# Kernel tuning notes

Hardware: AMD Instinct MI355X
Metric: run time of the kernel (lower is better)

## Reference

```python
import jax, jax.numpy as jnp
import numpy as np

B, D, CTX, H = 8192, 64, 256, 512  # batch, latent dim (made.nin), context dim, MADE hidden


def _masks(D, H):
    """Standard MADE natural-ordering masks (Germain et al. 2015)."""
    m0 = np.arange(1, D + 1)                 # input degrees 1..D
    mh = (np.arange(H) % (D - 1)) + 1        # hidden degrees 1..D-1
    M1 = (mh[:, None] >= m0[None, :]).astype(np.float32)   # (H, D)
    M2 = (mh[:, None] >= mh[None, :]).astype(np.float32)   # (H, H)
    mo = np.concatenate([m0, m0])            # outputs = [means; pre_scales]
    Mo = (mo[:, None] > mh[None, :]).astype(np.float32)    # (2D, H)
    return jnp.asarray(M1), jnp.asarray(M2), jnp.asarray(Mo)


def setup_inputs() -> dict:
    key = jax.random.key(0)
    ks = jax.random.split(key, 7)
    s = 0.05
    return {
        "context": jax.random.normal(ks[0], (B, CTX), jnp.float32),
        "eps": jax.random.normal(ks[1], (B, D), jnp.float32),  # reparameterization noise
        "W1": jax.random.normal(ks[2], (H, D), jnp.float32) * s,
        "b1": jnp.zeros((H,), jnp.float32),
        "Wc": jax.random.normal(ks[3], (H, CTX), jnp.float32) * s,
        "W2": jax.random.normal(ks[4], (H, H), jnp.float32) * s,
        "b2": jnp.zeros((H,), jnp.float32),
        "Wo": jax.random.normal(ks[5], (2 * D, H), jnp.float32) * s,
        "bo": jnp.zeros((2 * D,), jnp.float32),
    }


def reference(context, eps, W1, b1, Wc, W2, b2, Wo, bo):
    """AutoRegressiveDistribution.rsample (gaussian): D sequential MADE forwards,
    each extracting column i of (mu, softplus(pre_scale)) and sampling z_i."""
    M1, M2, Mo = _masks(D, H)
    W1m, W2m, Wom = (W1 * M1).T, (W2 * M2).T, (Wo * Mo).T
    ctx_h = context @ Wc.T  # context projection is constant across steps

    def step(z, i):
        h = jax.nn.relu(z @ W1m + ctx_h + b1)   # (B, H)
        h = jax.nn.relu(h @ W2m + b2)           # (B, H)
        out = h @ Wom + bo                      # (B, 2D): [means | pre_scales]
        mu_i = out[:, i]
        scale_i = jax.nn.softplus(out[:, D + i])
        z_i = mu_i + scale_i * eps[:, i]        # Normal(mu, scale).rsample()
        z = z.at[:, i].set(z_i)
        return z, (mu_i, scale_i)

    z0 = jnp.zeros((context.shape[0], D), context.dtype)
    z, (mus, scales) = jax.lax.scan(step, z0, jnp.arange(D))
    # state = (z_sample, mu_inferred, scale_inferred), each (B, D)
    return z, mus.T, scales.T
```

## Files before the change

kernel.cpp:

```cpp
#include <hip/hip_runtime.h>
#include <math.h>


typedef float f2 __attribute__((ext_vector_type(2)));

#define Bn 8192
#define Dn 64
#define CTXn 256
#define Hn 512
#define Rn 16

#define WQ_SZ  (64 * 512 * 12)
#define WOQ_SZ (64 * 64 * 20)
#define WCP_SZ (CTXn * Hn)

#define BARRIER() do {                                      \
    asm volatile("s_waitcnt lgkmcnt(0)" ::: "memory");      \
    __builtin_amdgcn_s_barrier();                           \
    asm volatile("" ::: "memory");                          \
  } while (0)

__device__ __forceinline__ int perm_of(int p, int* degout) {
  int k, t;
  if (p < 72) { k = p / 9 + 1; t = p - (k - 1) * 9; }
  else        { int pp = p - 72; k = pp / 8 + 9; t = pp - (k - 9) * 8; }
  *degout = k;
  return (k - 1) + 63 * t;
}
__device__ __forceinline__ int inv_perm(int h) {
  int i = h % 63;
  int t = h / 63;
  int base = (i < 9) ? 9 * i : 72 + 8 * (i - 8);
  return base + t;
}

#define R0e 262144
#define R1e (R0e + 32768)
#define R2e (R1e + 65536)
#define R3e (R2e + 131072)
#define R4e (R3e + 35840)
#define R5e (R4e + 1024)
__global__ void prep_kernel(const float* __restrict__ W1, const float* __restrict__ Wc,
                            const float* __restrict__ W2, const float* __restrict__ Wo,
                            const float* __restrict__ b1, const float* __restrict__ b2,
                            float* __restrict__ Wq, float* __restrict__ Woq,
                            float* __restrict__ WcpT, float* __restrict__ b1p,
                            float* __restrict__ b2p) {
  int idx = blockIdx.x * 256 + threadIdx.x;
  if (idx < R0e) {
    int hq = idx >> 9, hp = idx & 511;
    int i = hp % 63, e = hp / 63;
    Wq[i * 6144 + inv_perm(hq) * 12 + e] = W2[idx];
  } else if (idx < R1e) {
    int jj = idx - R0e;
    int hq = jj >> 6, i = jj & 63;
    Wq[i * 6144 + inv_perm(hq) * 12 + 9] = W1[jj];
  } else if (idx < R2e) {
    int jj = idx - R1e;
    int o = jj >> 9, hp = jj & 511;
    int i = hp % 63, p = hp / 63;
    int j = o & 63, half = o >> 6;
    Woq[i * 1280 + j * 20 + half * 10 + p] = Wo[jj];
  } else if (idx < R3e) {
    int jj = idx - R2e;
    int hq = jj >> 8, cc = jj & 255;
    int p = inv_perm(hq);
    int slot = (p < 256) ? (2 * p) : (2 * (p - 256) + 1);
    WcpT[cc * 512 + slot] = Wc[jj];
  } else if (idx < R4e) {
    int z = idx - R3e;
    if (z < 28672) {
      int i = 8 + (z >> 9), q = z & 511;
      Wq[i * 6144 + q * 12 + 8] = 0.f;
    } else {
      int z2 = z - 28672;
      int i = 8 + (z2 >> 7), r = z2 & 127;
      int j = r & 63, half = r >> 6;
      Woq[i * 1280 + j * 20 + half * 10 + 8] = 0.f;
    }
  } else if (idx < R5e) {
    int z = idx - R4e;
    if (z < 512) {
      int dq; int hq = perm_of(z, &dq);
      b1p[z] = b1[hq];
    } else {
      int q = z - 512;
      int dq; int hq = perm_of(q, &dq);
      b2p[q] = b2[hq];
    }
  }
}

__global__ __launch_bounds__(256, 2)
void made_pk_kernel(
    const float* __restrict__ context, const float* __restrict__ WcpT,
    const float* __restrict__ b1p,
    const float* __restrict__ Wq, const float* __restrict__ Woq,
    const float* __restrict__ b2p, const float* __restrict__ bo,
    const float* __restrict__ eps, float* __restrict__ out) {
  __shared__ __align__(16) float ctxR[Rn][264];
  __shared__ __align__(16) float zcur[16];
  __shared__ __align__(16) float h1g[9][16];
  __shared__ __align__(16) float h2g[9][16];

  int t = threadIdx.x;
  int b0 = blockIdx.x * Rn;
  int rp = t >> 6, l = t & 63;
  int q0 = t, q1 = t + 256;

  int g0 = ((q0 < 72) ? q0 / 9 + 1 : (q0 - 72) / 8 + 9) - 1;
  int g1 = ((q1 - 72) / 8 + 9) - 1;
  int qm = t | 63;
  int gm0s = __builtin_amdgcn_readfirstlane(
      ((qm < 72) ? qm / 9 + 1 : (qm - 72) / 8 + 9) - 1);
  int gm1s = __builtin_amdgcn_readfirstlane(((qm + 256 - 72) / 8 + 9) - 1);

  #pragma unroll
  for (int r = 0; r < Rn; ++r)
    ctxR[r][t] = context[(b0 + r) * CTXn + t];
  BARRIER();

  f2 accu[16];
  {
    f2 bias = (f2){b1p[q0], b1p[q1]};
    #pragma unroll
    for (int r = 0; r < 16; ++r) accu[r] = bias;
  }
  {
    const float* wc = WcpT + 2 * t;
    #pragma clang loop unroll(disable)
    for (int c4 = 0; c4 < CTXn / 4; ++c4) {
      f2 wv0 = *(const f2*)&wc[0];
      f2 wv1 = *(const f2*)&wc[Hn];
      f2 wv2 = *(const f2*)&wc[2 * Hn];
      f2 wv3 = *(const f2*)&wc[3 * Hn];
      wc += 4 * Hn;
      #pragma unroll
      for (int hf = 0; hf < 2; ++hf) {
        float4 x[8];
        #pragma unroll
        for (int r = 0; r < 8; ++r) x[r] = *(const float4*)&ctxR[8 * hf + r][4 * c4];
        #pragma unroll
        for (int r = 0; r < 8; ++r) {
          accu[8 * hf + r] += (f2){x[r].x, x[r].x} * wv0;
          accu[8 * hf + r] += (f2){x[r].y, x[r].y} * wv1;
          accu[8 * hf + r] += (f2){x[r].z, x[r].z} * wv2;
          accu[8 * hf + r] += (f2){x[r].w, x[r].w} * wv3;
        }
      }
    }
  }

  f2 a10[8], a11[8], a20[8], a21[8];
  #pragma unroll
  for (int r2 = 0; r2 < 8; ++r2) {
    a10[r2] = (f2){accu[2 * r2].x, accu[2 * r2 + 1].x};
    a11[r2] = (f2){accu[2 * r2].y, accu[2 * r2 + 1].y};
  }
  {
    float bb0 = b2p[q0], bb1 = b2p[q1];
    #pragma unroll
    for (int r2 = 0; r2 < 8; ++r2) {
      a20[r2] = (f2){bb0, bb0};
      a21[r2] = (f2){bb1, bb1};
    }
  }

  f2 ocA[2], ocB[2];
  ocA[0] = ocA[1] = (f2){bo[l], bo[l]};
  ocB[0] = ocB[1] = (f2){bo[l + 64], bo[l + 64]};
  int r0 = b0 + 4 * rp;
  f2 ez01 = (f2){eps[(r0 + 0) * Dn + l], eps[(r0 + 1) * Dn + l]};
  f2 ez23 = (f2){eps[(r0 + 2) * Dn + l], eps[(r0 + 3) * Dn + l]};
  f2 zs01 = (f2){0.f, 0.f}, zs23 = zs01;
  f2 mus01 = zs01, mus23 = zs01, scs01 = zs01, scs23 = zs01;

  const float* wq0p = Wq + (size_t)q0 * 12;
  const float* wq1p = Wq + (size_t)q1 * 12;
  const float* wopp = Woq + (size_t)l * 20;

  #pragma clang loop unroll(disable)
  for (int i = 0; i < Dn; ++i) {
    if (l == i) {
      f2 p01 = ocB[0], p23 = ocB[1];
      float s0 = fmaxf(p01.x, 0.f) + __logf(1.f + __expf(-fabsf(p01.x)));
      float s1 = fmaxf(p01.y, 0.f) + __logf(1.f + __expf(-fabsf(p01.y)));
      float s2 = fmaxf(p23.x, 0.f) + __logf(1.f + __expf(-fabsf(p23.x)));
      float s3 = fmaxf(p23.y, 0.f) + __logf(1.f + __expf(-fabsf(p23.y)));
      f2 sc01 = (f2){s0, s1}, sc23 = (f2){s2, s3};
      f2 z01 = ocA[0] + sc01 * ez01;
      f2 z23 = ocA[1] + sc23 * ez23;
      float4 zq = {z01.x, z01.y, z23.x, z23.y};
      *(float4*)&zcur[4 * rp] = zq;
      zs01 = z01; zs23 = z23;
      mus01 = ocA[0]; mus23 = ocA[1];
      scs01 = sc01; scs23 = sc23;
    }
    BARRIER();

    int sb = (i < 8) ? 9 * i : 8 * i + 8;
    bool liveB = (i <= gm1s);
    bool liveA = (i <= gm0s);
    float4 A1c0, A1c1, A1c2, A0c0, A0c1, A0c2;
    if (liveB) {
      const float4* a4 = (const float4*)wq1p;
      A1c0 = a4[0]; A1c1 = a4[1]; A1c2 = a4[2];
      if (liveA) {
        const float4* b4 = (const float4*)wq0p;
        A0c0 = b4[0]; A0c1 = b4[1]; A0c2 = b4[2];
      }
      float4 za = *(const float4*)&zcur[0];
      float4 zb = *(const float4*)&zcur[4];
      float4 zc = *(const float4*)&zcur[8];
      float4 zd = *(const float4*)&zcur[12];
      f2 zz[8] = {(f2){za.x, za.y}, (f2){za.z, za.w},
                  (f2){zb.x, zb.y}, (f2){zb.z, zb.w},
                  (f2){zc.x, zc.y}, (f2){zc.z, zc.w},
                  (f2){zd.x, zd.y}, (f2){zd.z, zd.w}};
      {
        f2 wv = (f2){A1c2.y, A1c2.y};
        #pragma unroll
        for (int r2 = 0; r2 < 8; ++r2) a11[r2] += wv * zz[r2];
        if (g1 == i) {
          int pp = q1 - sb;
          #pragma unroll
          for (int s = 0; s < 4; ++s) {
            float4 h = {fmaxf(a11[2 * s].x, 0.f), fmaxf(a11[2 * s].y, 0.f),
                        fmaxf(a11[2 * s + 1].x, 0.f), fmaxf(a11[2 * s + 1].y, 0.f)};
            *(float4*)&h1g[pp][4 * s] = h;
          }
        }
      }
      if (liveA) {
        f2 wv = (f2){A0c2.y, A0c2.y};
        #pragma unroll
        for (int r2 = 0; r2 < 8; ++r2) a10[r2] += wv * zz[r2];
        if (g0 == i) {
          int pp = q0 - sb;
          #pragma unroll
          for (int s = 0; s < 4; ++s) {
            float4 h = {fmaxf(a10[2 * s].x, 0.f), fmaxf(a10[2 * s].y, 0.f),
                        fmaxf(a10[2 * s + 1].x, 0.f), fmaxf(a10[2 * s + 1].y, 0.f)};
            *(float4*)&h1g[pp][4 * s] = h;
          }
        }
      }
    }
    BARRIER();

    const float4* w4 = (const float4*)wopp;
    float4 B0 = w4[0], B1 = w4[1], B2_ = w4[2], B3 = w4[3], B4 = w4[4];

    if (liveB) {
      float wA1[9] = {A1c0.x, A1c0.y, A1c0.z, A1c0.w,
                      A1c1.x, A1c1.y, A1c1.z, A1c1.w, A1c2.x};
      if (liveA) {
        float wA0[9] = {A0c0.x, A0c0.y, A0c0.z, A0c0.w,
                        A0c1.x, A0c1.y, A0c1.z, A0c1.w, A0c2.x};
        #pragma unroll
        for (int p = 0; p < 9; ++p) {
          float4 ha = *(const float4*)&h1g[p][0];
          float4 hb = *(const float4*)&h1g[p][4];
          float4 hc = *(const float4*)&h1g[p][8];
          float4 hd = *(const float4*)&h1g[p][12];
          f2 h[8] = {(f2){ha.x, ha.y}, (f2){ha.z, ha.w},
                     (f2){hb.x, hb.y}, (f2){hb.z, hb.w},
                     (f2){hc.x, hc.y}, (f2){hc.z, hc.w},
                     (f2){hd.x, hd.y}, (f2){hd.z, hd.w}};
          f2 wv1 = (f2){wA1[p], wA1[p]};
          f2 wv0 = (f2){wA0[p], wA0[p]};
          #pragma unroll
          for (int r2 = 0; r2 < 8; ++r2) {
            a21[r2] += wv1 * h[r2];
            a20[r2] += wv0 * h[r2];
          }
        }
      } else {
        #pragma unroll
        for (int p = 0; p < 9; ++p) {
          float4 ha = *(const float4*)&h1g[p][0];
          float4 hb = *(const float4*)&h1g[p][4];
          float4 hc = *(const float4*)&h1g[p][8];
          float4 hd = *(const float4*)&h1g[p][12];
          f2 h[8] = {(f2){ha.x, ha.y}, (f2){ha.z, ha.w},
                     (f2){hb.x, hb.y}, (f2){hb.z, hb.w},
                     (f2){hc.x, hc.y}, (f2){hc.z, hc.w},
                     (f2){hd.x, hd.y}, (f2){hd.z, hd.w}};
          f2 wv1 = (f2){wA1[p], wA1[p]};
          #pragma unroll
          for (int r2 = 0; r2 < 8; ++r2) a21[r2] += wv1 * h[r2];
        }
      }
      if (g1 == i) {
        int pp = q1 - sb;
        #pragma unroll
        for (int s = 0; s < 4; ++s) {
          float4 h = {fmaxf(a21[2 * s].x, 0.f), fmaxf(a21[2 * s].y, 0.f),
                      fmaxf(a21[2 * s + 1].x, 0.f), fmaxf(a21[2 * s + 1].y, 0.f)};
          *(float4*)&h2g[pp][4 * s] = h;
        }
      }
      if (liveA && g0 == i) {
        int pp = q0 - sb;
        #pragma unroll
        for (int s = 0; s < 4; ++s) {
          float4 h = {fmaxf(a20[2 * s].x, 0.f), fmaxf(a20[2 * s].y, 0.f),
                      fmaxf(a20[2 * s + 1].x, 0.f), fmaxf(a20[2 * s + 1].y, 0.f)};
          *(float4*)&h2g[pp][4 * s] = h;
        }
      }
    }
    BARRIER();

    {
      float wBa[9] = {B0.x, B0.y, B0.z, B0.w, B1.x, B1.y, B1.z, B1.w, B2_.x};
      float wBb[9] = {B2_.z, B2_.w, B3.x, B3.y, B3.z, B3.w, B4.x, B4.y, B4.z};
      #pragma unroll
      for (int p = 0; p < 9; ++p) {
        float4 hq = *(const float4*)&h2g[p][4 * rp];
        f2 h01 = (f2){hq.x, hq.y}, h23 = (f2){hq.z, hq.w};
        f2 wa = (f2){wBa[p], wBa[p]}, wb = (f2){wBb[p], wBb[p]};
        ocA[0] += wa * h01; ocA[1] += wa * h23;
        ocB[0] += wb * h01; ocB[1] += wb * h23;
      }
    }
    wq0p += 6144; wq1p += 6144; wopp += 1280;
  }

  out[(r0 + 0) * Dn + l] = zs01.x;
  out[(r0 + 1) * Dn + l] = zs01.y;
  out[(r0 + 2) * Dn + l] = zs23.x;
  out[(r0 + 3) * Dn + l] = zs23.y;
  out[Bn * Dn + (r0 + 0) * Dn + l] = mus01.x;
  out[Bn * Dn + (r0 + 1) * Dn + l] = mus01.y;
  out[Bn * Dn + (r0 + 2) * Dn + l] = mus23.x;
  out[Bn * Dn + (r0 + 3) * Dn + l] = mus23.y;
  out[2 * Bn * Dn + (r0 + 0) * Dn + l] = scs01.x;
  out[2 * Bn * Dn + (r0 + 1) * Dn + l] = scs01.y;
  out[2 * Bn * Dn + (r0 + 2) * Dn + l] = scs23.x;
  out[2 * Bn * Dn + (r0 + 3) * Dn + l] = scs23.y;
}

extern "C" void kernel_launch(void* const* d_in, const int* in_sizes, int n_in,
                              void* d_out, int out_size, void* d_ws, size_t ws_size,
                              hipStream_t stream) {
  const float* context = (const float*)d_in[0];
  const float* eps     = (const float*)d_in[1];
  const float* W1      = (const float*)d_in[2];
  const float* b1      = (const float*)d_in[3];
  const float* Wc      = (const float*)d_in[4];
  const float* W2      = (const float*)d_in[5];
  const float* b2      = (const float*)d_in[6];
  const float* Wo      = (const float*)d_in[7];
  const float* bo      = (const float*)d_in[8];
  float* out = (float*)d_out;

  float* ws   = (float*)d_ws;
  float* Wq   = ws;
  float* Woq  = Wq + WQ_SZ;
  float* WcpT = Woq + WOQ_SZ;
  float* b1p  = WcpT + WCP_SZ;
  float* b2p  = b1p + 512;

  prep_kernel<<<(R5e + 255) / 256, 256, 0, stream>>>(
      W1, Wc, W2, Wo, b1, b2, Wq, Woq, WcpT, b1p, b2p);
  made_pk_kernel<<<Bn / Rn, 256, 0, stream>>>(context, WcpT, b1p, Wq, Woq,
                                              b2p, bo, eps, out);
}
```

Before: 237.2 us.

## Add a critical-path wave to pipeline the sequential MADE step across 320 threads

Adds a fifth wavefront per block that owns the serial dependency chain: it computes z_i, the newly enabled hidden units of layers 1 and 2, and the output column for the current step. It relies on partial sums published by the four bulk waves through double-buffered LDS. The bulk waves now accumulate contributions one step behind, so the per-step chain shrinks to a single barrier instead of three, and the bulk GEMV work overlaps the critical path. In exchange, the critical wave recomputes the two most recent steps' contributions redundantly, the block grows to 320 threads, and LDS use and register pressure both rise.

```diff
diff --git a/kernel.cpp b/kernel.cpp
--- a/kernel.cpp
+++ b/kernel.cpp
@@ -9,6 +9,7 @@
 #define CTXn 256
 #define Hn 512
 #define Rn 16
+#define BD (Bn * Dn)
 
 #define WQ_SZ  (64 * 512 * 12)
 #define WOQ_SZ (64 * 64 * 20)
@@ -18,6 +19,10 @@
     asm volatile("s_waitcnt lgkmcnt(0)" ::: "memory");      \
     __builtin_amdgcn_s_barrier();                           \
     asm volatile("" ::: "memory");                          \
+  } while (0)
+
+#define WAVE_LDS_FENCE() do {                               \
+    asm volatile("s_waitcnt lgkmcnt(0)" ::: "memory");      \
   } while (0)
 
 __device__ __forceinline__ int perm_of(int p, int* degout) {
@@ -91,7 +96,7 @@
   }
 }
 
-__global__ __launch_bounds__(256, 2)
+__global__ __launch_bounds__(320, 2)
 void made_pk_kernel(
     const float* __restrict__ context, const float* __restrict__ WcpT,
     const float* __restrict__ b1p,
@@ -99,246 +104,365 @@
     const float* __restrict__ b2p, const float* __restrict__ bo,
     const float* __restrict__ eps, float* __restrict__ out) {
   __shared__ __align__(16) float ctxR[Rn][264];
-  __shared__ __align__(16) float zcur[16];
-  __shared__ __align__(16) float h1g[9][16];
-  __shared__ __align__(16) float h2g[9][16];
+  __shared__ __align__(16) float zpub[2][16];
+  __shared__ __align__(16) float h1pub[2][9][16];
+  __shared__ __align__(16) float h2pub[2][9][16];
+  __shared__ __align__(16) float a1h[2][9][16];
+  __shared__ __align__(16) float a2h[2][9][16];
+  __shared__ __align__(16) float och[2][32];
 
   int t = threadIdx.x;
   int b0 = blockIdx.x * Rn;
-  int rp = t >> 6, l = t & 63;
-  int q0 = t, q1 = t + 256;
-
-  int g0 = ((q0 < 72) ? q0 / 9 + 1 : (q0 - 72) / 8 + 9) - 1;
-  int g1 = ((q1 - 72) / 8 + 9) - 1;
-  int qm = t | 63;
-  int gm0s = __builtin_amdgcn_readfirstlane(
-      ((qm < 72) ? qm / 9 + 1 : (qm - 72) / 8 + 9) - 1);
-  int gm1s = __builtin_amdgcn_readfirstlane(((qm + 256 - 72) / 8 + 9) - 1);
-
-  #pragma unroll
-  for (int r = 0; r < Rn; ++r)
-    ctxR[r][t] = context[(b0 + r) * CTXn + t];
-  BARRIER();
-
-  f2 accu[16];
-  {
-    f2 bias = (f2){b1p[q0], b1p[q1]};
+
+  if (t < 256) {
+    int rp = t >> 6, l = t & 63;
+    int q0 = t, q1 = t + 256;
+    int g0 = ((q0 < 72) ? q0 / 9 + 1 : (q0 - 72) / 8 + 9) - 1;
+    int g1 = ((q1 - 72) / 8 + 9) - 1;
+    int qm = t | 63;
+    int gm0s = __builtin_amdgcn_readfirstlane(
+        ((qm < 72) ? qm / 9 + 1 : (qm - 72) / 8 + 9) - 1);
+    int gm1s = __builtin_amdgcn_readfirstlane(((qm + 256 - 72) / 8 + 9) - 1);
+
     #pragma unroll
-    for (int r = 0; r < 16; ++r) accu[r] = bias;
-  }
-  {
-    const float* wc = WcpT + 2 * t;
-    #pragma clang loop unroll(disable)
-    for (int c4 = 0; c4 < CTXn / 4; ++c4) {
-      f2 wv0 = *(const f2*)&wc[0];
-      f2 wv1 = *(const f2*)&wc[Hn];
-      f2 wv2 = *(const f2*)&wc[2 * Hn];
-      f2 wv3 = *(const f2*)&wc[3 * Hn];
-      wc += 4 * Hn;
+    for (int r = 0; r < Rn; ++r)
+      ctxR[r][t] = context[(b0 + r) * CTXn + t];
+    BARRIER();
+
+    f2 accu[16];
+    {
+      f2 bias = (f2){b1p[q0], b1p[q1]};
       #pragma unroll
-      for (int hf = 0; hf < 2; ++hf) {
-        float4 x[8];
+      for (int r = 0; r < 16; ++r) accu[r] = bias;
+    }
+    {
+      const float* wc = WcpT + 2 * t;
+      #pragma clang loop unroll(disable)
+      for (int c4 = 0; c4 < CTXn / 4; ++c4) {
+        f2 wv0 = *(const f2*)&wc[0];
+        f2 wv1 = *(const f2*)&wc[Hn];
+        f2 wv2 = *(const f2*)&wc[2 * Hn];
+        f2 wv3 = *(const f2*)&wc[3 * Hn];
+        wc += 4 * Hn;
         #pragma unroll
-        for (int r = 0; r < 8; ++r) x[r] = *(const float4*)&ctxR[8 * hf + r][4 * c4];
-        #pragma unroll
-        for (int r = 0; r < 8; ++r) {
-          accu[8 * hf + r] += (f2){x[r].x, x[r].x} * wv0;
-          accu[8 * hf + r] += (f2){x[r].y, x[r].y} * wv1;
-          accu[8 * hf + r] += (f2){x[r].z, x[r].z} * wv2;
-          accu[8 * hf + r] += (f2){x[r].w, x[r].w} * wv3;
-        }
-      }
-    }
-  }
-
-  f2 a10[8], a11[8], a20[8], a21[8];
-  #pragma unroll
-  for (int r2 = 0; r2 < 8; ++r2) {
-    a10[r2] = (f2){accu[2 * r2].x, accu[2 * r2 + 1].x};
-    a11[r2] = (f2){accu[2 * r2].y, accu[2 * r2 + 1].y};
-  }
-  {
-    float bb0 = b2p[q0], bb1 = b2p[q1];
+        for (int hf = 0; hf < 2; ++hf) {
+          float4 x[8];
+          #pragma unroll
+          for (int r = 0; r < 8; ++r) x[r] = *(const float4*)&ctxR[8 * hf + r][4 * c4];
+          #pragma unroll
+          for (int r = 0; r < 8; ++r) {
+            accu[8 * hf + r] += (f2){x[r].x, x[r].x} * wv0;
+            accu[8 * hf + r] += (f2){x[r].y, x[r].y} * wv1;
+            accu[8 * hf + r] += (f2){x[r].z, x[r].z} * wv2;
+            accu[8 * hf + r] += (f2){x[r].w, x[r].w} * wv3;
+          }
+        }
+      }
+    }
+    f2 a10[8], a11[8], a20[8], a21[8];
     #pragma unroll
     for (int r2 = 0; r2 < 8; ++r2) {
-      a20[r2] = (f2){bb0, bb0};
-      a21[r2] = (f2){bb1, bb1};
+      a10[r2] = (f2){accu[2 * r2].x, accu[2 * r2 + 1].x};
+      a11[r2] = (f2){accu[2 * r2].y, accu[2 * r2 + 1].y};
+    }
+    {
+      float bb0 = b2p[q0], bb1 = b2p[q1];
+      #pragma unroll
+      for (int r2 = 0; r2 < 8; ++r2) {
+        a20[r2] = (f2){bb0, bb0};
+        a21[r2] = (f2){bb1, bb1};
+      }
+    }
+    f2 ocA[2], ocB[2];
+    ocA[0] = ocA[1] = (f2){bo[l], bo[l]};
+    ocB[0] = ocB[1] = (f2){bo[l + 64], bo[l + 64]};
+
+    if (g0 == 0) {
+      int pp = q0;
+      #pragma unroll
+      for (int s = 0; s < 4; ++s) {
+        *(float4*)&a1h[1][pp][4 * s] =
+            (float4){a10[2 * s].x, a10[2 * s].y, a10[2 * s + 1].x, a10[2 * s + 1].y};
+        *(float4*)&a2h[1][pp][4 * s] =
+            (float4){a20[2 * s].x, a20[2 * s].y, a20[2 * s + 1].x, a20[2 * s + 1].y};
+      }
+    }
+    if (l == 0) {
+      *(float4*)&och[1][4 * rp] =
+          (float4){ocA[0].x, ocA[0].y, ocA[1].x, ocA[1].y};
+      *(float4*)&och[1][16 + 4 * rp] =
+          (float4){ocB[0].x, ocB[0].y, ocB[1].x, ocB[1].y};
+    }
+    BARRIER();
+
+    #pragma clang loop unroll(disable)
+    for (int S = 0; S < Dn; ++S) {
+      if (S >= 1) {
+        int i = S - 1;
+        int pb = i & 1;
+        int sbp = (i < 8) ? 9 * i : 8 * i + 8;
+        (void)sbp;
+        bool liveB = (i <= gm1s);
+        bool liveA = (i <= gm0s);
+        const float* wq0p = Wq + (size_t)i * 6144 + (size_t)q0 * 12;
+        const float* wq1p = Wq + (size_t)i * 6144 + (size_t)q1 * 12;
+        const float* wopp = Woq + (size_t)i * 1280 + (size_t)l * 20;
+        const float4* w4 = (const float4*)wopp;
+        float4 B0 = w4[0], B1 = w4[1], B2_ = w4[2], B3 = w4[3], B4 = w4[4];
+
+        if (liveB) {
+          const float4* a4 = (const float4*)wq1p;
+          float4 A1c0 = a4[0], A1c1 = a4[1], A1c2 = a4[2];
+          float4 A0c0, A0c1, A0c2;
+          if (liveA) {
+            const float4* b4 = (const float4*)wq0p;
+            A0c0 = b4[0]; A0c1 = b4[1]; A0c2 = b4[2];
+          }
+          float4 za = *(const float4*)&zpub[pb][0];
+          float4 zb = *(const float4*)&zpub[pb][4];
+          float4 zc = *(const float4*)&zpub[pb][8];
+          float4 zd = *(const float4*)&zpub[pb][12];
+          f2 zz[8] = {(f2){za.x, za.y}, (f2){za.z, za.w},
+                      (f2){zb.x, zb.y}, (f2){zb.z, zb.w},
+                      (f2){zc.x, zc.y}, (f2){zc.z, zc.w},
+                      (f2){zd.x, zd.y}, (f2){zd.z, zd.w}};
+          {
+            f2 wv = (f2){A1c2.y, A1c2.y};
+            #pragma unroll
+            for (int r2 = 0; r2 < 8; ++r2) a11[r2] += wv * zz[r2];
+          }
+          if (liveA) {
+            f2 wv = (f2){A0c2.y, A0c2.y};
+            #pragma unroll
+            for (int r2 = 0; r2 < 8; ++r2) a10[r2] += wv * zz[r2];
+          }
+          float wA1[9] = {A1c0.x, A1c0.y, A1c0.z, A1c0.w,
+                          A1c1.x, A1c1.y, A1c1.z, A1c1.w, A1c2.x};
+          if (liveA) {
+            float wA0[9] = {A0c0.x, A0c0.y, A0c0.z, A0c0.w,
+                            A0c1.x, A0c1.y, A0c1.z, A0c1.w, A0c2.x};
+            #pragma unroll
+            for (int p = 0; p < 9; ++p) {
+              float4 ha = *(const float4*)&h1pub[pb][p][0];
+              float4 hb = *(const float4*)&h1pub[pb][p][4];
+              float4 hc = *(const float4*)&h1pub[pb][p][8];
+              float4 hd = *(const float4*)&h1pub[pb][p][12];
+              f2 h[8] = {(f2){ha.x, ha.y}, (f2){ha.z, ha.w},
+                         (f2){hb.x, hb.y}, (f2){hb.z, hb.w},
+                         (f2){hc.x, hc.y}, (f2){hc.z, hc.w},
+                         (f2){hd.x, hd.y}, (f2){hd.z, hd.w}};
+              f2 wv1 = (f2){wA1[p], wA1[p]};
+              f2 wv0 = (f2){wA0[p], wA0[p]};
+              #pragma unroll
+              for (int r2 = 0; r2 < 8; ++r2) {
+                a21[r2] += wv1 * h[r2];
+                a20[r2] += wv0 * h[r2];
+              }
+            }
+          } else {
+            #pragma unroll
+            for (int p = 0; p < 9; ++p) {
+              float4 ha = *(const float4*)&h1pub[pb][p][0];
+              float4 hb = *(const float4*)&h1pub[pb][p][4];
+              float4 hc = *(const float4*)&h1pub[pb][p][8];
+              float4 hd = *(const float4*)&h1pub[pb][p][12];
+              f2 h[8] = {(f2){ha.x, ha.y}, (f2){ha.z, ha.w},
+                         (f2){hb.x, hb.y}, (f2){hb.z, hb.w},
+                         (f2){hc.x, hc.y}, (f2){hc.z, hc.w},
+                         (f2){hd.x, hd.y}, (f2){hd.z, hd.w}};
+              f2 wv1 = (f2){wA1[p], wA1[p]};
+              #pragma unroll
+              for (int r2 = 0; r2 < 8; ++r2) a21[r2] += wv1 * h[r2];
+            }
+          }
+        }
+        {
+          float wBa[9] = {B0.x, B0.y, B0.z, B0.w, B1.x, B1.y, B1.z, B1.w, B2_.x};
+          float wBb[9] = {B2_.z, B2_.w, B3.x, B3.y, B3.z, B3.w, B4.x, B4.y, B4.z};
+          #pragma unroll
+          for (int p = 0; p < 9; ++p) {
+            float4 hq = *(const float4*)&h2pub[pb][p][4 * rp];
+            f2 h01 = (f2){hq.x, hq.y}, h23 = (f2){hq.z, hq.w};
+            f2 wa = (f2){wBa[p], wBa[p]}, wb = (f2){wBb[p], wBb[p]};
+            ocA[0] += wa * h01; ocA[1] += wa * h23;
+            ocB[0] += wb * h01; ocB[1] += wb * h23;
+          }
+        }
+      }
+
+      int ph = S & 1;
+      if (S + 1 <= 62) {
+        int sb1 = (S + 1 < 8) ? 9 * (S + 1) : 8 * (S + 1) + 8;
+        if (g1 == S + 1) {
+          int pp = q1 - sb1;
+          #pragma unroll
+          for (int s = 0; s < 4; ++s) {
+            *(float4*)&a1h[ph][pp][4 * s] =
+                (float4){a11[2 * s].x, a11[2 * s].y, a11[2 * s + 1].x, a11[2 * s + 1].y};
+            *(float4*)&a2h[ph][pp][4 * s] =
+                (float4){a21[2 * s].x, a21[2 * s].y, a21[2 * s + 1].x, a21[2 * s + 1].y};
+          }
+        }
+        if (g0 == S + 1) {
+          int pp = q0 - sb1;
+          #pragma unroll
+          for (int s = 0; s < 4; ++s) {
+            *(float4*)&a1h[ph][pp][4 * s] =
+                (float4){a10[2 * s].x, a10[2 * s].y, a10[2 * s + 1].x, a10[2 * s + 1].y};
+            *(float4*)&a2h[ph][pp][4 * s] =
+                (float4){a20[2 * s].x, a20[2 * s].y, a20[2 * s + 1].x, a20[2 * s + 1].y};
+          }
+        }
+      }
+      if (S + 1 <= 63 && l == S + 1) {
+        *(float4*)&och[ph][4 * rp] =
+            (float4){ocA[0].x, ocA[0].y, ocA[1].x, ocA[1].y};
+        *(float4*)&och[ph][16 + 4 * rp] =
+            (float4){ocB[0].x, ocB[0].y, ocB[1].x, ocB[1].y};
+      }
+      BARRIER();
+    }
+  } else {
+    int l = t & 63;
+    int r = l & 15;
+    int jA = l >> 4;
+    bool lo16 = (l < 16);
+
+    BARRIER();
+    BARRIER();
+
+    #pragma clang loop unroll(disable)
+    for (int sc = 0; sc < Dn; ++sc) {
+      int p = sc & 1, pn = p ^ 1;
+      int sb = (sc < 8) ? 9 * sc : 8 * sc + 8;
+      bool has9 = (sc < 8);
+      bool fin = (sc <= 62);
+
+      float4 Ca0 = {}, Ca1 = {}, Ca2 = {}, Cb0 = {}, Cb1 = {}, Cb2 = {};
+      float4 Pa0 = {}, Pa1 = {}, Pa2 = {}, Pb0 = {}, Pb1 = {}, Pb2 = {};
+      float4 Cc0 = {}, Cc1 = {}, Cc2 = {}, Pc0 = {}, Pc1 = {}, Pc2 = {};
+      if (fin) {
+        int qA = sb + jA, qB = qA + 4;
+        const float4* ca = (const float4*)(Wq + (size_t)sc * 6144 + (size_t)qA * 12);
+        Ca0 = ca[0]; Ca1 = ca[1]; Ca2 = ca[2];
+        const float4* cb = (const float4*)(Wq + (size_t)sc * 6144 + (size_t)qB * 12);
+        Cb0 = cb[0]; Cb1 = cb[1]; Cb2 = cb[2];
+        if (sc >= 1) {
+          const float4* pa = (const float4*)(Wq + (size_t)(sc - 1) * 6144 + (size_t)qA * 12);
+          Pa0 = pa[0]; Pa1 = pa[1]; Pa2 = pa[2];
+          const float4* pb_ = (const float4*)(Wq + (size_t)(sc - 1) * 6144 + (size_t)qB * 12);
+          Pb0 = pb_[0]; Pb1 = pb_[1]; Pb2 = pb_[2];
+        }
+        if (has9 && lo16) {
+          int qC = sb + 8;
+          const float4* cc = (const float4*)(Wq + (size_t)sc * 6144 + (size_t)qC * 12);
+          Cc0 = cc[0]; Cc1 = cc[1]; Cc2 = cc[2];
+          if (sc >= 1) {
+            const float4* pc = (const float4*)(Wq + (size_t)(sc - 1) * 6144 + (size_t)qC * 12);
+            Pc0 = pc[0]; Pc1 = pc[1]; Pc2 = pc[2];
+          }
+        }
+      }
+      float woA[9], woB[9];
+      float epsv = 0.f;
+      if (lo16) {
+        epsv = eps[(b0 + r) * Dn + sc];
+        if (sc >= 1) {
+          const float4* wo = (const float4*)(Woq + (size_t)(sc - 1) * 1280 + (size_t)sc * 20);
+          float4 W0 = wo[0], W1_ = wo[1], W2v = wo[2], W3 = wo[3], W4 = wo[4];
+          woA[0] = W0.x; woA[1] = W0.y; woA[2] = W0.z; woA[3] = W0.w;
+          woA[4] = W1_.x; woA[5] = W1_.y; woA[6] = W1_.z; woA[7] = W1_.w;
+          woA[8] = W2v.x;
+          woB[0] = W2v.z; woB[1] = W2v.w; woB[2] = W3.x; woB[3] = W3.y;
+          woB[4] = W3.z; woB[5] = W3.w; woB[6] = W4.x; woB[7] = W4.y;
+          woB[8] = W4.z;
+        }
+      }
+
+      if (lo16) {
+        float ocAv = och[pn][r];
+        float ocBv = och[pn][16 + r];
+        if (sc >= 1) {
+          #pragma unroll
+          for (int k = 0; k < 9; ++k) {
+            float h2v = h2pub[pn][k][r];
+            ocAv = fmaf(woA[k], h2v, ocAv);
+            ocBv = fmaf(woB[k], h2v, ocBv);
+          }
+        }
+        float sp = fmaxf(ocBv, 0.f) + __logf(1.f + __expf(-fabsf(ocBv)));
+        float z = ocAv + sp * epsv;
+        zpub[p][r] = z;
+        out[(b0 + r) * Dn + sc] = z;
+        out[BD + (b0 + r) * Dn + sc] = ocAv;
+        out[2 * BD + (b0 + r) * Dn + sc] = sp;
+      }
+      WAVE_LDS_FENCE();
+
+      if (fin) {
+        float zc = zpub[p][r];
+        float zp = (sc >= 1) ? zpub[pn][r] : 0.f;
+        {
+          float a1A = a1h[pn][jA][r] + Ca2.y * zc + Pa2.y * zp;
+          h1pub[p][jA][r] = fmaxf(a1A, 0.f);
+          float a1B = a1h[pn][jA + 4][r] + Cb2.y * zc + Pb2.y * zp;
+          h1pub[p][jA + 4][r] = fmaxf(a1B, 0.f);
+          if (has9 && lo16) {
+            float a1C = a1h[pn][8][r] + Cc2.y * zc + Pc2.y * zp;
+            h1pub[p][8][r] = fmaxf(a1C, 0.f);
+          }
+        }
+        WAVE_LDS_FENCE();
+        {
+          float hc[9], hp[9];
+          #pragma unroll
+          for (int k = 0; k < 9; ++k) hc[k] = h1pub[p][k][r];
+          if (sc >= 1) {
+            #pragma unroll
+            for (int k = 0; k < 9; ++k) hp[k] = h1pub[pn][k][r];
+          } else {
+            #pragma unroll
+            for (int k = 0; k < 9; ++k) hp[k] = 0.f;
+          }
+          float wcA[9] = {Ca0.x, Ca0.y, Ca0.z, Ca0.w,
+                          Ca1.x, Ca1.y, Ca1.z, Ca1.w, Ca2.x};
+          float wpA[9] = {Pa0.x, Pa0.y, Pa0.z, Pa0.w,
+                          Pa1.x, Pa1.y, Pa1.z, Pa1.w, Pa2.x};
+          float a2A = a2h[pn][jA][r];
+          #pragma unroll
+          for (int k = 0; k < 9; ++k) a2A = fmaf(wcA[k], hc[k], a2A);
+          #pragma unroll
+          for (int k = 0; k < 9; ++k) a2A = fmaf(wpA[k], hp[k], a2A);
+          h2pub[p][jA][r] = fmaxf(a2A, 0.f);
+
+          float wcB[9] = {Cb0.x, Cb0.y, Cb0.z, Cb0.w,
+                          Cb1.x, Cb1.y, Cb1.z, Cb1.w, Cb2.x};
+          float wpB[9] = {Pb0.x, Pb0.y, Pb0.z, Pb0.w,
+                          Pb1.x, Pb1.y, Pb1.z, Pb1.w, Pb2.x};
+          float a2B = a2h[pn][jA + 4][r];
+          #pragma unroll
+          for (int k = 0; k < 9; ++k) a2B = fmaf(wcB[k], hc[k], a2B);
+          #pragma unroll
+          for (int k = 0; k < 9; ++k) a2B = fmaf(wpB[k], hp[k], a2B);
+          h2pub[p][jA + 4][r] = fmaxf(a2B, 0.f);
+
+          if (has9 && lo16) {
+            float wcC[9] = {Cc0.x, Cc0.y, Cc0.z, Cc0.w,
+                            Cc1.x, Cc1.y, Cc1.z, Cc1.w, Cc2.x};
+            float wpC[9] = {Pc0.x, Pc0.y, Pc0.z, Pc0.w,
+                            Pc1.x, Pc1.y, Pc1.z, Pc1.w, Pc2.x};
+            float a2C = a2h[pn][8][r];
+            #pragma unroll
+            for (int k = 0; k < 9; ++k) a2C = fmaf(wcC[k], hc[k], a2C);
+            #pragma unroll
+            for (int k = 0; k < 9; ++k) a2C = fmaf(wpC[k], hp[k], a2C);
+            h2pub[p][8][r] = fmaxf(a2C, 0.f);
+          }
+        }
+      }
+      BARRIER();
     }
   }
-
-  f2 ocA[2], ocB[2];
-  ocA[0] = ocA[1] = (f2){bo[l], bo[l]};
-  ocB[0] = ocB[1] = (f2){bo[l + 64], bo[l + 64]};
-  int r0 = b0 + 4 * rp;
-  f2 ez01 = (f2){eps[(r0 + 0) * Dn + l], eps[(r0 + 1) * Dn + l]};
-  f2 ez23 = (f2){eps[(r0 + 2) * Dn + l], eps[(r0 + 3) * Dn + l]};
-  f2 zs01 = (f2){0.f, 0.f}, zs23 = zs01;
-  f2 mus01 = zs01, mus23 = zs01, scs01 = zs01, scs23 = zs01;
-
-  const float* wq0p = Wq + (size_t)q0 * 12;
-  const float* wq1p = Wq + (size_t)q1 * 12;
-  const float* wopp = Woq + (size_t)l * 20;
-
-  #pragma clang loop unroll(disable)
-  for (int i = 0; i < Dn; ++i) {
-    if (l == i) {
-      f2 p01 = ocB[0], p23 = ocB[1];
-      float s0 = fmaxf(p01.x, 0.f) + __logf(1.f + __expf(-fabsf(p01.x)));
-      float s1 = fmaxf(p01.y, 0.f) + __logf(1.f + __expf(-fabsf(p01.y)));
-      float s2 = fmaxf(p23.x, 0.f) + __logf(1.f + __expf(-fabsf(p23.x)));
-      float s3 = fmaxf(p23.y, 0.f) + __logf(1.f + __expf(-fabsf(p23.y)));
-      f2 sc01 = (f2){s0, s1}, sc23 = (f2){s2, s3};
-      f2 z01 = ocA[0] + sc01 * ez01;
-      f2 z23 = ocA[1] + sc23 * ez23;
-      float4 zq = {z01.x, z01.y, z23.x, z23.y};
-      *(float4*)&zcur[4 * rp] = zq;
-      zs01 = z01; zs23 = z23;
-      mus01 = ocA[0]; mus23 = ocA[1];
-      scs01 = sc01; scs23 = sc23;
-    }
-    BARRIER();
-
-    int sb = (i < 8) ? 9 * i : 8 * i + 8;
-    bool liveB = (i <= gm1s);
-    bool liveA = (i <= gm0s);
-    float4 A1c0, A1c1, A1c2, A0c0, A0c1, A0c2;
-    if (liveB) {
-      const float4* a4 = (const float4*)wq1p;
-      A1c0 = a4[0]; A1c1 = a4[1]; A1c2 = a4[2];
-      if (liveA) {
-        const float4* b4 = (const float4*)wq0p;
-        A0c0 = b4[0]; A0c1 = b4[1]; A0c2 = b4[2];
-      }
-      float4 za = *(const float4*)&zcur[0];
-      float4 zb = *(const float4*)&zcur[4];
-      float4 zc = *(const float4*)&zcur[8];
-      float4 zd = *(const float4*)&zcur[12];
-      f2 zz[8] = {(f2){za.x, za.y}, (f2){za.z, za.w},
-                  (f2){zb.x, zb.y}, (f2){zb.z, zb.w},
-                  (f2){zc.x, zc.y}, (f2){zc.z, zc.w},
-                  (f2){zd.x, zd.y}, (f2){zd.z, zd.w}};
-      {
-        f2 wv = (f2){A1c2.y, A1c2.y};
-        #pragma unroll
-        for (int r2 = 0; r2 < 8; ++r2) a11[r2] += wv * zz[r2];
-        if (g1 == i) {
-          int pp = q1 - sb;
-          #pragma unroll
-          for (int s = 0; s < 4; ++s) {
-            float4 h = {fmaxf(a11[2 * s].x, 0.f), fmaxf(a11[2 * s].y, 0.f),
-                        fmaxf(a11[2 * s + 1].x, 0.f), fmaxf(a11[2 * s + 1].y, 0.f)};
-            *(float4*)&h1g[pp][4 * s] = h;
-          }
-        }
-      }
-      if (liveA) {
-        f2 wv = (f2){A0c2.y, A0c2.y};
-        #pragma unroll
-        for (int r2 = 0; r2 < 8; ++r2) a10[r2] += wv * zz[r2];
-        if (g0 == i) {
-          int pp = q0 - sb;
-          #pragma unroll
-          for (int s = 0; s < 4; ++s) {
-            float4 h = {fmaxf(a10[2 * s].x, 0.f), fmaxf(a10[2 * s].y, 0.f),
-                        fmaxf(a10[2 * s + 1].x, 0.f), fmaxf(a10[2 * s + 1].y, 0.f)};
-            *(float4*)&h1g[pp][4 * s] = h;
-          }
-        }
-      }
-    }
-    BARRIER();
-
-    const float4* w4 = (const float4*)wopp;
-    float4 B0 = w4[0], B1 = w4[1], B2_ = w4[2], B3 = w4[3], B4 = w4[4];
-
-    if (liveB) {
-      float wA1[9] = {A1c0.x, A1c0.y, A1c0.z, A1c0.w,
-                      A1c1.x, A1c1.y, A1c1.z, A1c1.w, A1c2.x};
-      if (liveA) {
-        float wA0[9] = {A0c0.x, A0c0.y, A0c0.z, A0c0.w,
-                        A0c1.x, A0c1.y, A0c1.z, A0c1.w, A0c2.x};
-        #pragma unroll
-        for (int p = 0; p < 9; ++p) {
-          float4 ha = *(const float4*)&h1g[p][0];
-          float4 hb = *(const float4*)&h1g[p][4];
-          float4 hc = *(const float4*)&h1g[p][8];
-          float4 hd = *(const float4*)&h1g[p][12];
-          f2 h[8] = {(f2){ha.x, ha.y}, (f2){ha.z, ha.w},
-                     (f2){hb.x, hb.y}, (f2){hb.z, hb.w},
-                     (f2){hc.x, hc.y}, (f2){hc.z, hc.w},
-                     (f2){hd.x, hd.y}, (f2){hd.z, hd.w}};
-          f2 wv1 = (f2){wA1[p], wA1[p]};
-          f2 wv0 = (f2){wA0[p], wA0[p]};
-          #pragma unroll
-          for (int r2 = 0; r2 < 8; ++r2) {
-            a21[r2] += wv1 * h[r2];
-            a20[r2] += wv0 * h[r2];
-          }
-        }
-      } else {
-        #pragma unroll
-        for (int p = 0; p < 9; ++p) {
-          float4 ha = *(const float4*)&h1g[p][0];
-          float4 hb = *(const float4*)&h1g[p][4];
-          float4 hc = *(const float4*)&h1g[p][8];
-          float4 hd = *(const float4*)&h1g[p][12];
-          f2 h[8] = {(f2){ha.x, ha.y}, (f2){ha.z, ha.w},
-                     (f2){hb.x, hb.y}, (f2){hb.z, hb.w},
-                     (f2){hc.x, hc.y}, (f2){hc.z, hc.w},
-                     (f2){hd.x, hd.y}, (f2){hd.z, hd.w}};
-          f2 wv1 = (f2){wA1[p], wA1[p]};
-          #pragma unroll
-          for (int r2 = 0; r2 < 8; ++r2) a21[r2] += wv1 * h[r2];
-        }
-      }
-      if (g1 == i) {
-        int pp = q1 - sb;
-        #pragma unroll
-        for (int s = 0; s < 4; ++s) {
-          float4 h = {fmaxf(a21[2 * s].x, 0.f), fmaxf(a21[2 * s].y, 0.f),
-                      fmaxf(a21[2 * s + 1].x, 0.f), fmaxf(a21[2 * s + 1].y, 0.f)};
-          *(float4*)&h2g[pp][4 * s] = h;
-        }
-      }
-      if (liveA && g0 == i) {
-        int pp = q0 - sb;
-        #pragma unroll
-        for (int s = 0; s < 4; ++s) {
-          float4 h = {fmaxf(a20[2 * s].x, 0.f), fmaxf(a20[2 * s].y, 0.f),
-                      fmaxf(a20[2 * s + 1].x, 0.f), fmaxf(a20[2 * s + 1].y, 0.f)};
-          *(float4*)&h2g[pp][4 * s] = h;
-        }
-      }
-    }
-    BARRIER();
-
-    {
-      float wBa[9] = {B0.x, B0.y, B0.z, B0.w, B1.x, B1.y, B1.z, B1.w, B2_.x};
-      float wBb[9] = {B2_.z, B2_.w, B3.x, B3.y, B3.z, B3.w, B4.x, B4.y, B4.z};
-      #pragma unroll
-      for (int p = 0; p < 9; ++p) {
-        float4 hq = *(const float4*)&h2g[p][4 * rp];
-        f2 h01 = (f2){hq.x, hq.y}, h23 = (f2){hq.z, hq.w};
-        f2 wa = (f2){wBa[p], wBa[p]}, wb = (f2){wBb[p], wBb[p]};
-        ocA[0] += wa * h01; ocA[1] += wa * h23;
-        ocB[0] += wb * h01; ocB[1] += wb * h23;
-      }
-    }
-    wq0p += 6144; wq1p += 6144; wopp += 1280;
-  }
-
-  out[(r0 + 0) * Dn + l] = zs01.x;
-  out[(r0 + 1) * Dn + l] = zs01.y;
-  out[(r0 + 2) * Dn + l] = zs23.x;
-  out[(r0 + 3) * Dn + l] = zs23.y;
-  out[Bn * Dn + (r0 + 0) * Dn + l] = mus01.x;
-  out[Bn * Dn + (r0 + 1) * Dn + l] = mus01.y;
-  out[Bn * Dn + (r0 + 2) * Dn + l] = mus23.x;
-  out[Bn * Dn + (r0 + 3) * Dn + l] = mus23.y;
-  out[2 * Bn * Dn + (r0 + 0) * Dn + l] = scs01.x;
-  out[2 * Bn * Dn + (r0 + 1) * Dn + l] = scs01.y;
-  out[2 * Bn * Dn + (r0 + 2) * Dn + l] = scs23.x;
-  out[2 * Bn * Dn + (r0 + 3) * Dn + l] = scs23.y;
 }
 
 extern "C" void kernel_launch(void* const* d_in, const int* in_sizes, int n_in,
@@ -364,6 +488,6 @@
 
   prep_kernel<<<(R5e + 255) / 256, 256, 0, stream>>>(
       W1, Wc, W2, Wo, b1, b2, Wq, Woq, WcpT, b1p, b2p);
-  made_pk_kernel<<<Bn / Rn, 256, 0, stream>>>(context, WcpT, b1p, Wq, Woq,
+  made_pk_kernel<<<Bn / Rn, 320, 0, stream>>>(context, WcpT, b1p, Wq, Woq,
                                               b2p, bo, eps, out);
 }
```

Result: slower. 309.0 us (+30.2%).
